# Performance work log

Measured on AMD Instinct MI355X. Metric: run time of the kernel, lower is better.

## Reference

```python
import jax, jax.numpy as jnp
import numpy as np

IN_FEATURES = 3
OUT_FEATURES = 256
WEIGHT_SCALE = 1.0
ALPHA = 6.0


def setup_inputs() -> dict:
    key = jax.random.key(0)
    k_x, k_w, k_b, k_mu, k_g = jax.random.split(key, 5)
    B, N = 4, 65536
    # coordinates in [-1, 1], matching mu's init range
    x = jax.random.uniform(k_x, (B, N, IN_FEATURES), jnp.float32, -1.0, 1.0)
    # gamma ~ Gamma(alpha, 1)
    gamma = jax.random.gamma(k_g, ALPHA, (OUT_FEATURES,), jnp.float32)
    # linear weight init (Kaiming-uniform-like) then scaled by weight_scale * sqrt(gamma)
    bound = 1.0 / np.sqrt(IN_FEATURES)
    W = jax.random.uniform(k_w, (OUT_FEATURES, IN_FEATURES), jnp.float32, -bound, bound)
    W = W * (WEIGHT_SCALE * jnp.sqrt(gamma)[:, None])
    # bias ~ U(-pi, pi)
    b = jax.random.uniform(k_b, (OUT_FEATURES,), jnp.float32, -np.pi, np.pi)
    # mu ~ U(-1, 1), stored as (out, in) (the (1,1,out,in) singleton dims are pure broadcast)
    mu = jax.random.uniform(k_mu, (OUT_FEATURES, IN_FEATURES), jnp.float32, -1.0, 1.0)
    return {"x": x, "W": W, "b": b, "mu": mu, "gamma": gamma}


def reference(x, W, b, mu, gamma):
    # linear: (B, N, out)
    lin = jnp.einsum("bnd,od->bno", x, W) + b
    x2 = jnp.sum(x * x, axis=-1, keepdims=True)          # (B, N, 1)
    mu2 = jnp.sum(mu * mu, axis=-1)                       # (out,)
    cross = jnp.einsum("bnd,od->bno", x, mu)             # (B, N, out)
    D = x2 - 2.0 * cross + mu2                            # (B, N, out)
    return jnp.sin(lin) * jnp.exp(-0.5 * D * gamma)
```

## Files before the change

### kernel.cpp

```cpp
#include <hip/hip_runtime.h>


#define OUT_FEATURES 256

__global__ __launch_bounds__(256) void gabor_kernel(
    const float* __restrict__ x,
    const float* __restrict__ W,
    const float* __restrict__ b,
    const float* __restrict__ mu,
    const float* __restrict__ gamma,
    float* __restrict__ out,
    int P)
{
    const int lane        = threadIdx.x & 63;
    const int waveInBlock = threadIdx.x >> 6;
    const int wavesPerBlk = blockDim.x >> 6;
    const int waveId      = blockIdx.x * wavesPerBlk + waveInBlock;
    const int wavesTotal  = gridDim.x * wavesPerBlk;

    const int o = lane << 2;

    float w0[4], w1[4], w2[4], bb[4], m0[4], m1[4], m2[4], mu2s[4], gs[4];
#pragma unroll
    for (int j = 0; j < 4; ++j) {
        const int oj = o + j;
        w0[j] = W[oj * 3 + 0];
        w1[j] = W[oj * 3 + 1];
        w2[j] = W[oj * 3 + 2];
        m0[j] = mu[oj * 3 + 0];
        m1[j] = mu[oj * 3 + 1];
        m2[j] = mu[oj * 3 + 2];
        bb[j] = b[oj];
        gs[j] = -0.5f * gamma[oj];
        mu2s[j] = m0[j] * m0[j] + m1[j] * m1[j] + m2[j] * m2[j];
    }

    for (int p = waveId; p < P; p += wavesTotal) {
        const float x0 = x[p * 3 + 0];
        const float x1 = x[p * 3 + 1];
        const float x2 = x[p * 3 + 2];
        const float xs = x0 * x0 + x1 * x1 + x2 * x2;

        float4 r;
        float* rp = &r.x;
#pragma unroll
        for (int j = 0; j < 4; ++j) {
            const float lin   = fmaf(w0[j], x0, fmaf(w1[j], x1, fmaf(w2[j], x2, bb[j])));
            const float cross = fmaf(m0[j], x0, fmaf(m1[j], x1, m2[j] * x2));
            const float D     = xs - 2.0f * cross + mu2s[j];
            rp[j] = __sinf(lin) * __expf(gs[j] * D);
        }

        *reinterpret_cast<float4*>(out + (size_t)p * OUT_FEATURES + o) = r;
    }
}

extern "C" void kernel_launch(void* const* d_in, const int* in_sizes, int n_in,
                              void* d_out, int out_size, void* d_ws, size_t ws_size,
                              hipStream_t stream) {
    const float* x     = (const float*)d_in[0];
    const float* W     = (const float*)d_in[1];
    const float* b     = (const float*)d_in[2];
    const float* mu    = (const float*)d_in[3];
    const float* gamma = (const float*)d_in[4];
    float* out = (float*)d_out;

    const int P = in_sizes[0] / 3;

    const int blocks = 2048;
    gabor_kernel<<<blocks, 256, 0, stream>>>(x, W, b, mu, gamma, out, P);
}
```

Baseline: 283.0 us.

## Use contiguous per-wave point chunks, unroll by four, and nontemporal stores

Each wave now handles a contiguous range of points instead of a grid stride. It loads four points' coordinates at once and writes four output rows per iteration using nontemporal vector stores. The wave index is made scalar via readfirstlane, and the launch bounds ask for more occupancy. The goal is to cut cache pollution from the 256 MB write stream and improve store and load batching. The risk is that contiguous chunks per wave may spread concurrent writes across DRAM pages less evenly.

```diff
diff --git a/kernel.cpp b/kernel.cpp
--- a/kernel.cpp
+++ b/kernel.cpp
@@ -1,9 +1,11 @@
 #include <hip/hip_runtime.h>
 
 
-#define OUT_FEATURES 256
+#define OUT_F 256
 
-__global__ __launch_bounds__(256) void gabor_kernel(
+typedef float v4f __attribute__((ext_vector_type(4)));
+
+__global__ __launch_bounds__(256, 4) void gabor_kernel(
     const float* __restrict__ x,
     const float* __restrict__ W,
     const float* __restrict__ b,
@@ -15,8 +17,8 @@
     const int lane        = threadIdx.x & 63;
     const int waveInBlock = threadIdx.x >> 6;
     const int wavesPerBlk = blockDim.x >> 6;
-    const int waveId      = blockIdx.x * wavesPerBlk + waveInBlock;
     const int wavesTotal  = gridDim.x * wavesPerBlk;
+    const int waveId = __builtin_amdgcn_readfirstlane(blockIdx.x * wavesPerBlk + waveInBlock);
 
     const int o = lane << 2;
 
@@ -35,23 +37,49 @@
         mu2s[j] = m0[j] * m0[j] + m1[j] * m1[j] + m2[j] * m2[j];
     }
 
-    for (int p = waveId; p < P; p += wavesTotal) {
+    const int ppw  = (P + wavesTotal - 1) / wavesTotal;
+    const int p0   = waveId * ppw;
+    const int pend = (p0 + ppw < P) ? (p0 + ppw) : P;
+
+    int p = p0;
+    for (; p + 4 <= pend; p += 4) {
+        const float* xp = x + (size_t)p * 3;
+        float xv[12];
+#pragma unroll
+        for (int i = 0; i < 12; ++i) xv[i] = xp[i];
+
+        float* orow = out + (size_t)p * OUT_F + o;
+#pragma unroll
+        for (int q = 0; q < 4; ++q) {
+            const float x0 = xv[q * 3 + 0];
+            const float x1 = xv[q * 3 + 1];
+            const float x2 = xv[q * 3 + 2];
+            const float xs = x0 * x0 + x1 * x1 + x2 * x2;
+            v4f r;
+#pragma unroll
+            for (int j = 0; j < 4; ++j) {
+                const float lin   = fmaf(w0[j], x0, fmaf(w1[j], x1, fmaf(w2[j], x2, bb[j])));
+                const float cross = fmaf(m0[j], x0, fmaf(m1[j], x1, m2[j] * x2));
+                const float D     = xs - 2.0f * cross + mu2s[j];
+                r[j] = __sinf(lin) * __expf(gs[j] * D);
+            }
+            __builtin_nontemporal_store(r, (v4f*)(orow + (size_t)q * OUT_F));
+        }
+    }
+    for (; p < pend; ++p) {
         const float x0 = x[p * 3 + 0];
         const float x1 = x[p * 3 + 1];
         const float x2 = x[p * 3 + 2];
         const float xs = x0 * x0 + x1 * x1 + x2 * x2;
-
-        float4 r;
-        float* rp = &r.x;
+        v4f r;
 #pragma unroll
         for (int j = 0; j < 4; ++j) {
             const float lin   = fmaf(w0[j], x0, fmaf(w1[j], x1, fmaf(w2[j], x2, bb[j])));
             const float cross = fmaf(m0[j], x0, fmaf(m1[j], x1, m2[j] * x2));
             const float D     = xs - 2.0f * cross + mu2s[j];
-            rp[j] = __sinf(lin) * __expf(gs[j] * D);
+            r[j] = __sinf(lin) * __expf(gs[j] * D);
         }
-
-        *reinterpret_cast<float4*>(out + (size_t)p * OUT_FEATURES + o) = r;
+        __builtin_nontemporal_store(r, (v4f*)(out + (size_t)p * OUT_F + o));
     }
 }
 
@@ -67,6 +95,5 @@
 
     const int P = in_sizes[0] / 3;
 
-    const int blocks = 2048;
-    gabor_kernel<<<blocks, 256, 0, stream>>>(x, W, b, mu, gamma, out, P);
+    gabor_kernel<<<2048, 256, 0, stream>>>(x, W, b, mu, gamma, out, P);
 }
```

Result: no change. 282.4 us (-0.2%).
